# Kernel tuning notes

Hardware: AMD Instinct MI355X
Metric: run time of the kernel (lower is better)

## Reference

```python
import jax, jax.numpy as jnp
import numpy as np

D_MODEL = 1024
NUM_HEADS = 16
D_K = D_MODEL // NUM_HEADS
NEG_INF = -1.0e9


def setup_inputs() -> dict:
    key = jax.random.key(0)
    ks = jax.random.split(key, 12)
    B, S = 2, 2048
    s = 1.0 / np.sqrt(D_MODEL)
    return {
        "q": jax.random.normal(ks[0], (B, S, D_MODEL), jnp.float32),
        "k": jax.random.normal(ks[1], (B, S, D_MODEL), jnp.float32),
        "v": jax.random.normal(ks[2], (B, S, D_MODEL), jnp.float32),
        "encoder_mask": jnp.ones((B, 1, 1, S), jnp.int32),
        "W_q": jax.random.normal(ks[3], (D_MODEL, D_MODEL), jnp.float32) * s,
        "b_q": jnp.zeros((D_MODEL,), jnp.float32),
        "W_k": jax.random.normal(ks[4], (D_MODEL, D_MODEL), jnp.float32) * s,
        "b_k": jnp.zeros((D_MODEL,), jnp.float32),
        "W_v": jax.random.normal(ks[5], (D_MODEL, D_MODEL), jnp.float32) * s,
        "b_v": jnp.zeros((D_MODEL,), jnp.float32),
        "W_o": jax.random.normal(ks[6], (D_MODEL, D_MODEL), jnp.float32) * s,
        "b_o": jnp.zeros((D_MODEL,), jnp.float32),
    }


def reference(q, k, v, encoder_mask, W_q, b_q, W_k, b_k, W_v, b_v, W_o, b_o):
    B, S, _ = q.shape
    # projections (torch Linear: x @ W^T + b)
    def proj(x, W, b):
        y = x @ W.T + b
        return y.reshape(B, -1, NUM_HEADS, D_K).transpose(0, 2, 1, 3)  # [B,H,S,dk]

    Q = proj(q, W_q, b_q)
    K = proj(k, W_k, b_k)
    V = proj(v, W_v, b_v)

    scores = jnp.einsum("bhqd,bhkd->bhqk", Q, K) / jnp.sqrt(jnp.float32(D_K))
    scores = jnp.where(encoder_mask == 0, NEG_INF, scores)
    # NOTE: source module computes softmax(scores) but then (bug) multiplies
    # the raw masked scores by V; softmax result is dead code, so we skip it.
    attn_out = jnp.einsum("bhqk,bhkd->bhqd", scores, V)
    attn_out = attn_out.transpose(0, 2, 1, 3).reshape(B, S, D_MODEL)
    return attn_out @ W_o.T + b_o
```

## Files before the change

### kernel.cpp

```cpp
#include <hip/hip_runtime.h>
#include <stdint.h>

#define DM 1024
#define NH 16
#define DK 64

typedef __attribute__((ext_vector_type(8))) __bf16 bf16x8;
typedef __attribute__((ext_vector_type(4))) float f32x4;

__device__ __forceinline__ float bf2f(unsigned short u) {
    union { uint32_t i; float f; } x; x.i = ((uint32_t)u) << 16; return x.f;
}
__device__ __forceinline__ unsigned short f2bf(float f) {
    union { float f; uint32_t i; } x; x.f = f;
    uint32_t r = x.i + 0x7fffu + ((x.i >> 16) & 1u);
    return (unsigned short)(r >> 16);
}

__device__ __forceinline__ void gl2lds16(const void* g, void* l) {
    __builtin_amdgcn_global_load_lds(
        (const __attribute__((address_space(1))) void*)g,
        (__attribute__((address_space(3))) void*)l, 16, 0, 0);
}

__device__ __forceinline__ f32x4 mfma_bf16(bf16x8 a, bf16x8 b, f32x4 c) {
    return __builtin_amdgcn_mfma_f32_16x16x32_bf16(a, b, c, 0, 0, 0);
}

template<int N> __device__ __forceinline__ void waitvm() {
    if constexpr (N == 0) asm volatile("s_waitcnt vmcnt(0)" ::: "memory");
}

struct CvtArgs {
    const float* src[15];
    unsigned short* dst[15];
};

__global__ __launch_bounds__(256) void cvt15(CvtArgs a) {
    const int t = blockIdx.x * 256 + threadIdx.x;
    const int seg = t >> 18;
    const int off = t & 0x3ffff;
    const float4 v = reinterpret_cast<const float4*>(a.src[seg])[off];
    ushort4 o;
    o.x = f2bf(v.x); o.y = f2bf(v.y); o.z = f2bf(v.z); o.w = f2bf(v.w);
    reinterpret_cast<ushort4*>(a.dst[seg])[off] = o;
}

template<typename OutT>
struct GKArgs {
    const unsigned short* A[3];
    const unsigned short* Wlo[3];
    const unsigned short* Whi[3];
    const float* blo[3];
    const float* bhi[3];
    OutT* C[3];
};

template<int BM, int BN, typename OutT>
__global__ __launch_bounds__(256, 4) void gemmk(GKArgs<OutT> g, int M, int N, int K,
                                                int nwgx, int rowSplit)
{
    constexpr int SA = BM / 64;
    constexpr int SB = BN / 64;
    constexpr int FN = BN / 32;
    constexpr int BUFE = (BM + BN) * 32;
    constexpr int EPIE = BM * BN * (int)(sizeof(OutT) / 2);
    constexpr int LDSE = (2 * BUFE > EPIE) ? 2 * BUFE : EPIE;

    const int z = blockIdx.y;
    const int nwg = gridDim.x;
    const int f = blockIdx.x;
    const int q = nwg >> 3;
    const int f2 = (f & 7) * q + (f >> 3);
    const int bx = f2 % nwgx, by = f2 / nwgx;
    const int row0 = by * BM, col0 = bx * BN;

    const unsigned short* __restrict__ A = g.A[z];
    const bool hi = row0 >= rowSplit;
    const unsigned short* __restrict__ Bw = hi ? g.Whi[z] : g.Wlo[z];
    const float* __restrict__ bias = hi ? g.bhi[z] : g.blo[z];
    OutT* __restrict__ C = g.C[z];

    __shared__ unsigned short lds[LDSE];

    const int tid  = threadIdx.x;
    const int lane = tid & 63;
    const int w    = tid >> 6;
    const int wr   = w >> 1, wc = w & 1;
    const int l15  = lane & 15;
    const int swz  = (l15 & 12) << 2;

    const int tidp = tid ^ ((tid >> 4) & 3);
    const unsigned short* aSrc = A  + (size_t)(row0 + (tidp >> 2)) * K + (tidp & 3) * 8;
    const unsigned short* bSrc = Bw + (size_t)(col0 + (tidp >> 2)) * K + (tidp & 3) * 8;

    const int aBase = (((wr * 64 + l15) * 64) + (lane >> 4) * 16) ^ swz;
    const int bBase = (((wc * (BN / 2) + l15) * 64) + (lane >> 4) * 16) ^ swz;

    f32x4 acc[4][FN];
    #pragma unroll
    for (int m = 0; m < 4; ++m)
        #pragma unroll
        for (int n = 0; n < FN; ++n)
            acc[m][n] = (f32x4){0.f, 0.f, 0.f, 0.f};

    const int NT = K >> 5;

    #define STAGE(t) do { \
        unsigned short* bufE = lds + ((t) & 1) * BUFE; \
        _Pragma("unroll") \
        for (int i = 0; i < SA; ++i) \
            gl2lds16(aSrc + (size_t)(t) * 32 + (size_t)i * 64 * K, \
                     bufE + i * 2048 + tid * 8); \
        _Pragma("unroll") \
        for (int i = 0; i < SB; ++i) \
            gl2lds16(bSrc + (size_t)(t) * 32 + (size_t)i * 64 * K, \
                     bufE + BM * 32 + i * 2048 + tid * 8); \
    } while (0)

    STAGE(0);
    waitvm<0>();
    __builtin_amdgcn_s_barrier();

    #pragma unroll 2
    for (int t = 0; t < NT; ++t) {
        if (t + 1 < NT) STAGE(t + 1);
        const char* LA = (const char*)lds + (t & 1) * (BUFE * 2);
        const char* LB = LA + BM * 64;
        bf16x8 af[4], bfv[FN];
        #pragma unroll
        for (int m = 0; m < 4; ++m)
            af[m] = *reinterpret_cast<const bf16x8*>(LA + m * 1024 + aBase);
        #pragma unroll
        for (int n = 0; n < FN; ++n)
            bfv[n] = *reinterpret_cast<const bf16x8*>(LB + n * 1024 + bBase);
        __builtin_amdgcn_s_setprio(1);
        #pragma unroll
        for (int m = 0; m < 4; ++m)
            #pragma unroll
            for (int n = 0; n < FN; ++n)
                acc[m][n] = mfma_bf16(af[m], bfv[n], acc[m][n]);
        __builtin_amdgcn_s_setprio(0);
        if (t + 1 < NT) waitvm<0>();
        __builtin_amdgcn_s_barrier();
    }
    #undef STAGE

    const int cr = (lane >> 4) * 4, cc = l15;
    if constexpr (sizeof(OutT) == 2) {
        unsigned short* CE = lds;
        #pragma unroll
        for (int n = 0; n < FN; ++n) {
            const int col = wc * (BN / 2) + n * 16 + cc;
            const float bv = bias[col0 + col];
            #pragma unroll
            for (int m = 0; m < 4; ++m) {
                const int rowb = wr * 64 + m * 16 + cr;
                #pragma unroll
                for (int r = 0; r < 4; ++r)
                    CE[(rowb + r) * BN + col] = f2bf(acc[m][n][r] + bv);
            }
        }
        __syncthreads();
        constexpr int NJ = BM * BN * 2 / 4096;
        #pragma unroll
        for (int j = 0; j < NJ; ++j) {
            const int off = j * 4096 + tid * 16;
            const int row = off / (BN * 2);
            const int cole = (off % (BN * 2)) >> 1;
            *reinterpret_cast<uint4*>(&C[(size_t)(row0 + row) * N + col0 + cole]) =
                *reinterpret_cast<const uint4*>((const char*)CE + off);
        }
    } else {
        float* CE = reinterpret_cast<float*>(lds);
        #pragma unroll
        for (int n = 0; n < FN; ++n) {
            const int col = wc * (BN / 2) + n * 16 + cc;
            const float bv = bias[col0 + col];
            #pragma unroll
            for (int m = 0; m < 4; ++m) {
                const int rowb = wr * 64 + m * 16 + cr;
                #pragma unroll
                for (int r = 0; r < 4; ++r)
                    CE[(rowb + r) * BN + col] = acc[m][n][r] + bv;
            }
        }
        __syncthreads();
        constexpr int NJ = BM * BN * 4 / 4096;
        #pragma unroll
        for (int j = 0; j < NJ; ++j) {
            const int off = j * 4096 + tid * 16;
            const int row = off / (BN * 4);
            const int cole = (off % (BN * 4)) >> 2;
            *reinterpret_cast<uint4*>(&C[(size_t)(row0 + row) * N + col0 + cole]) =
                *reinterpret_cast<const uint4*>((const char*)CE + off);
        }
    }
}

__global__ __launch_bounds__(256) void ktv_partial(
    const unsigned short* __restrict__ Kb, const unsigned short* __restrict__ Vb,
    const int* __restrict__ mask, float* __restrict__ Mpart,
    float* __restrict__ cvpart, int S, int schunk)
{
    __shared__ float Ks[16][64];
    __shared__ float Vs[16][64];
    __shared__ float cvs[16][64];
    const int bh = blockIdx.x, chunk = blockIdx.y, BH = gridDim.x;
    const int b = bh >> 4, h = bh & 15;
    const int tid = threadIdx.x;
    const int tx = tid & 15, ty = tid >> 4;
    const int s0 = chunk * schunk;

    float acc[4][4] = {};
    float cv[4] = {0.f, 0.f, 0.f, 0.f};

    for (int sc = 0; sc < schunk; sc += 16) {
        const int s = s0 + sc + ty;
        const size_t rowoff = (size_t)(b * S + s) * DM + h * DK + tx * 4;
        const ushort4 kraw = *reinterpret_cast<const ushort4*>(Kb + rowoff);
        const ushort4 vraw = *reinterpret_cast<const ushort4*>(Vb + rowoff);
        float4 kv = make_float4(bf2f(kraw.x), bf2f(kraw.y), bf2f(kraw.z), bf2f(kraw.w));
        const float4 vv = make_float4(bf2f(vraw.x), bf2f(vraw.y), bf2f(vraw.z), bf2f(vraw.w));
        if (mask[b * S + s] == 0) {
            cv[0] += vv.x; cv[1] += vv.y; cv[2] += vv.z; cv[3] += vv.w;
            kv = make_float4(0.f, 0.f, 0.f, 0.f);
        }
        __syncthreads();
        *reinterpret_cast<float4*>(&Ks[ty][tx * 4]) = kv;
        *reinterpret_cast<float4*>(&Vs[ty][tx * 4]) = vv;
        __syncthreads();
        #pragma unroll
        for (int ss = 0; ss < 16; ++ss) {
            const float4 kq = *reinterpret_cast<const float4*>(&Ks[ss][ty * 4]);
            const float4 vq = *reinterpret_cast<const float4*>(&Vs[ss][tx * 4]);
            const float kvv[4] = {kq.x, kq.y, kq.z, kq.w};
            const float vvv[4] = {vq.x, vq.y, vq.z, vq.w};
            #pragma unroll
            for (int i = 0; i < 4; ++i)
                #pragma unroll
                for (int j = 0; j < 4; ++j)
                    acc[i][j] += kvv[i] * vvv[j];
        }
    }

    const size_t mbase = ((size_t)chunk * BH + bh) * (DK * DK);
    #pragma unroll
    for (int i = 0; i < 4; ++i)
        #pragma unroll
        for (int j = 0; j < 4; ++j)
            Mpart[mbase + (size_t)(ty * 4 + i) * DK + tx * 4 + j] = acc[i][j];

    __syncthreads();
    #pragma unroll
    for (int j = 0; j < 4; ++j) cvs[ty][tx * 4 + j] = cv[j];
    __syncthreads();
    if (tid < DK) {
        float s = 0.f;
        #pragma unroll
        for (int r = 0; r < 16; ++r) s += cvs[r][tid];
        cvpart[((size_t)chunk * BH + bh) * DK + tid] = s;
    }
}

__global__ __launch_bounds__(256) void reduce_m(
    const float* __restrict__ Mpart, const float* __restrict__ cvpart,
    float* __restrict__ Mm, float* __restrict__ cvec, int nchunk, int BH)
{
    const int bh = blockIdx.x;
    const int tid = threadIdx.x;
    const int e0 = blockIdx.y * 512;
    for (int e = e0 + tid; e < e0 + 512; e += 256) {
        float s = 0.f;
        for (int c = 0; c < nchunk; ++c)
            s += Mpart[((size_t)c * BH + bh) * (DK * DK) + e];
        Mm[(size_t)bh * DK * DK + e] = s * 0.125f;
    }
    if (blockIdx.y == 0 && tid < DK) {
        float s = 0.f;
        for (int c = 0; c < nchunk; ++c)
            s += cvpart[((size_t)c * BH + bh) * DK + tid];
        cvec[bh * DK + tid] = s;
    }
}

__device__ __forceinline__ bf16x8 ld_cvt8(const float* p) {
    const float4 x = *reinterpret_cast<const float4*>(p);
    const float4 y = *reinterpret_cast<const float4*>(p + 4);
    union { unsigned short u[8]; bf16x8 v; } r;
    r.u[0] = f2bf(x.x); r.u[1] = f2bf(x.y); r.u[2] = f2bf(x.z); r.u[3] = f2bf(x.w);
    r.u[4] = f2bf(y.x); r.u[5] = f2bf(y.y); r.u[6] = f2bf(y.z); r.u[7] = f2bf(y.w);
    return r.v;
}

__global__ __launch_bounds__(256) void fuse_w(
    const float* __restrict__ Mm, const float* __restrict__ Wo,
    unsigned short* __restrict__ Wf)
{
    const int h = blockIdx.y;
    const int b = blockIdx.z;
    const int o0 = blockIdx.x * 256;
    const int tid = threadIdx.x, lane = tid & 63, w = tid >> 6;
    const int l15 = lane & 15, q8 = (lane >> 4) * 8;
    const float* MmH = Mm + (size_t)(b * NH + h) * (DK * DK);

    f32x4 acc[4][4];
    #pragma unroll
    for (int m = 0; m < 4; ++m)
        #pragma unroll
        for (int n = 0; n < 4; ++n)
            acc[m][n] = (f32x4){0.f, 0.f, 0.f, 0.f};

    bf16x8 af[4][2], bf[4][2];
    #pragma unroll
    for (int m = 0; m < 4; ++m) {
        const int orow = o0 + w * 64 + m * 16 + l15;
        #pragma unroll
        for (int kk = 0; kk < 2; ++kk)
            af[m][kk] = ld_cvt8(Wo + (size_t)orow * DM + h * DK + kk * 32 + q8);
    }
    #pragma unroll
    for (int n = 0; n < 4; ++n) {
        const int d = n * 16 + l15;
        #pragma unroll
        for (int kk = 0; kk < 2; ++kk)
            bf[n][kk] = ld_cvt8(MmH + (size_t)d * DK + kk * 32 + q8);
    }
    #pragma unroll
    for (int kk = 0; kk < 2; ++kk)
        #pragma unroll
        for (int m = 0; m < 4; ++m)
            #pragma unroll
            for (int n = 0; n < 4; ++n)
                acc[m][n] = mfma_bf16(af[m][kk], bf[n][kk], acc[m][n]);

    const int cr = (lane >> 4) * 4, cc = lane & 15;
    #pragma unroll
    for (int n = 0; n < 4; ++n)
        #pragma unroll
        for (int m = 0; m < 4; ++m)
            #pragma unroll
            for (int r = 0; r < 4; ++r)
                Wf[(size_t)b * DM * DM +
                   (size_t)(o0 + w * 64 + m * 16 + cr + r) * DM +
                   h * DK + n * 16 + cc] = f2bf(acc[m][n][r]);
}

__global__ __launch_bounds__(256) void fuse_bias(
    const float* __restrict__ cvec, const float* __restrict__ Wo,
    const float* __restrict__ bo, float* __restrict__ bias2)
{
    const int w = threadIdx.x >> 6, lane = threadIdx.x & 63;
    const int o = blockIdx.x * 4 + w;
    const float* wr = Wo + (size_t)o * DM + lane * 16;
    const float* c0 = cvec + lane * 16;
    const float* c1 = cvec + DM + lane * 16;
    float s0 = 0.f, s1 = 0.f;
    #pragma unroll
    for (int u = 0; u < 4; ++u) {
        const float4 w4 = *reinterpret_cast<const float4*>(wr + u * 4);
        const float4 a4 = *reinterpret_cast<const float4*>(c0 + u * 4);
        const float4 b4 = *reinterpret_cast<const float4*>(c1 + u * 4);
        s0 += w4.x * a4.x + w4.y * a4.y + w4.z * a4.z + w4.w * a4.w;
        s1 += w4.x * b4.x + w4.y * b4.y + w4.z * b4.z + w4.w * b4.w;
    }
    #pragma unroll
    for (int d = 32; d >= 1; d >>= 1) {
        s0 += __shfl_xor(s0, d, 64);
        s1 += __shfl_xor(s1, d, 64);
    }
    if (lane == 0) {
        const float bv = bo[o];
        bias2[o]      = bv - 1.0e9f * s0;
        bias2[DM + o] = bv - 1.0e9f * s1;
    }
}

extern "C" void kernel_launch(void* const* d_in, const int* in_sizes, int n_in,
                              void* d_out, int out_size, void* d_ws, size_t ws_size,
                              hipStream_t stream)
{
    const float* q    = (const float*)d_in[0];
    const float* k    = (const float*)d_in[1];
    const float* v    = (const float*)d_in[2];
    const int*   mask = (const int*)  d_in[3];
    const float* Wq   = (const float*)d_in[4];
    const float* bq   = (const float*)d_in[5];
    const float* Wk   = (const float*)d_in[6];
    const float* bk   = (const float*)d_in[7];
    const float* Wv   = (const float*)d_in[8];
    const float* bv   = (const float*)d_in[9];
    const float* Wo   = (const float*)d_in[10];
    const float* bo   = (const float*)d_in[11];
    float* out = (float*)d_out;

    const int BS = in_sizes[0] / DM;
    const int B  = 2;
    const int S  = BS / B;
    const int BH = B * NH;
    const int SCHUNK = 64;
    const int NCHUNK = S / SCHUNK;
    const size_t BSDM = (size_t)BS * DM;
    const size_t DMDM = (size_t)DM * DM;

    unsigned short* ws = (unsigned short*)d_ws;
    unsigned short* qb   = ws;
    unsigned short* kb   = qb  + BSDM;
    unsigned short* vb   = kb  + BSDM;
    unsigned short* Wqb  = vb  + BSDM;
    unsigned short* Wkb  = Wqb + DMDM;
    unsigned short* Wvb  = Wkb + DMDM;
    unsigned short* Qp   = Wvb + DMDM;
    unsigned short* Kp   = Qp  + BSDM;
    unsigned short* Vp   = Kp  + BSDM;
    float* Mpart = (float*)kb;
    float* cvprt = (float*)Wqb;
    float* Mm    = cvprt + (size_t)NCHUNK * BH * DK;
    float* cvec  = Mm    + (size_t)BH * DK * DK;
    unsigned short* Wf = qb;
    float* bias2 = (float*)Wkb;

    const dim3 blk(256);

    CvtArgs cv;
    for (int i = 0; i < 4; ++i) { cv.src[0 + i] = q + (size_t)i * DMDM; cv.dst[0 + i] = qb + (size_t)i * DMDM; }
    for (int i = 0; i < 4; ++i) { cv.src[4 + i] = k + (size_t)i * DMDM; cv.dst[4 + i] = kb + (size_t)i * DMDM; }
    for (int i = 0; i < 4; ++i) { cv.src[8 + i] = v + (size_t)i * DMDM; cv.dst[8 + i] = vb + (size_t)i * DMDM; }
    cv.src[12] = Wq; cv.dst[12] = Wqb;
    cv.src[13] = Wk; cv.dst[13] = Wkb;
    cv.src[14] = Wv; cv.dst[14] = Wvb;
    cvt15<<<dim3(15 * 1024), blk, 0, stream>>>(cv);

    GKArgs<unsigned short> ga;
    ga.A[0] = qb;  ga.A[1] = kb;  ga.A[2] = vb;
    ga.Wlo[0] = ga.Whi[0] = Wqb;
    ga.Wlo[1] = ga.Whi[1] = Wkb;
    ga.Wlo[2] = ga.Whi[2] = Wvb;
    ga.blo[0] = ga.bhi[0] = bq;
    ga.blo[1] = ga.bhi[1] = bk;
    ga.blo[2] = ga.bhi[2] = bv;
    ga.C[0] = Qp;  ga.C[1] = Kp;  ga.C[2] = Vp;
    gemmk<128, 128, unsigned short>
        <<<dim3((DM / 128) * (BS / 128), 3), blk, 0, stream>>>(
        ga, BS, DM, DM, DM / 128, 1 << 30);

    ktv_partial<<<dim3(BH, NCHUNK), blk, 0, stream>>>(Kp, Vp, mask, Mpart, cvprt, S, SCHUNK);
    reduce_m<<<dim3(BH, 8), blk, 0, stream>>>(Mpart, cvprt, Mm, cvec, NCHUNK, BH);

    fuse_w<<<dim3(DM / 256, NH, B), blk, 0, stream>>>(Mm, Wo, Wf);
    fuse_bias<<<dim3(DM / 4), blk, 0, stream>>>(cvec, Wo, bo, bias2);

    GKArgs<float> gf;
    gf.A[0] = Qp;
    gf.Wlo[0] = Wf;        gf.Whi[0] = Wf + DMDM;
    gf.blo[0] = bias2;     gf.bhi[0] = bias2 + DM;
    gf.C[0] = out;
    gf.A[1] = gf.A[2] = nullptr;
    gf.Wlo[1] = gf.Wlo[2] = gf.Whi[1] = gf.Whi[2] = nullptr;
    gf.blo[1] = gf.blo[2] = gf.bhi[1] = gf.bhi[2] = nullptr;
    gf.C[1] = gf.C[2] = nullptr;
    gemmk<128, 64, float>
        <<<dim3((DM / 64) * (BS / 128), 1), blk, 0, stream>>>(
        gf, BS, DM, DM, DM / 64, S);
}
```

Measured before the change: 118.9 us.

## Fuse fp32-to-bf16 activation conversion into QKV projection GEMM A-tile staging

The separate conversion pass over q, k and v is removed. The QKV GEMM now streams fp32 activations straight into LDS with a new swizzle and converts them to bf16 when loading fragments. This avoids writing and re-reading a bf16 copy of the activations, but it doubles the A-tile LDS footprint and global read bytes per tile and adds conversion ALU work in the inner loop. Occupancy launch bounds drop from 4 to 3, and the workspace layout is reorganised.

```diff
diff --git a/kernel.cpp b/kernel.cpp
--- a/kernel.cpp
+++ b/kernel.cpp
@@ -32,11 +32,11 @@
 }
 
 struct CvtArgs {
-    const float* src[15];
-    unsigned short* dst[15];
+    const float* src[3];
+    unsigned short* dst[3];
 };
 
-__global__ __launch_bounds__(256) void cvt15(CvtArgs a) {
+__global__ __launch_bounds__(256) void cvt3(CvtArgs a) {
     const int t = blockIdx.x * 256 + threadIdx.x;
     const int seg = t >> 18;
     const int off = t & 0x3ffff;
@@ -48,7 +48,7 @@
 
 template<typename OutT>
 struct GKArgs {
-    const unsigned short* A[3];
+    const void* A[3];
     const unsigned short* Wlo[3];
     const unsigned short* Whi[3];
     const float* blo[3];
@@ -56,16 +56,17 @@
     OutT* C[3];
 };
 
-template<int BM, int BN, typename OutT>
-__global__ __launch_bounds__(256, 4) void gemmk(GKArgs<OutT> g, int M, int N, int K,
+template<int BM, int BN, bool F32A, typename OutT>
+__global__ __launch_bounds__(256, 3) void gemmk(GKArgs<OutT> g, int M, int N, int K,
                                                 int nwgx, int rowSplit)
 {
-    constexpr int SA = BM / 64;
+    static_assert(!F32A || BM == 128, "F32A staging hardcodes BM=128");
     constexpr int SB = BN / 64;
     constexpr int FN = BN / 32;
-    constexpr int BUFE = (BM + BN) * 32;
-    constexpr int EPIE = BM * BN * (int)(sizeof(OutT) / 2);
-    constexpr int LDSE = (2 * BUFE > EPIE) ? 2 * BUFE : EPIE;
+    constexpr int ABYTES = F32A ? BM * 128 : BM * 64;
+    constexpr int BUFE   = ABYTES / 2 + BN * 32;
+    constexpr int EPIE   = BM * BN * (int)(sizeof(OutT) / 2);
+    constexpr int LDSE   = (2 * BUFE > EPIE) ? 2 * BUFE : EPIE;
 
     const int z = blockIdx.y;
     const int nwg = gridDim.x;
@@ -75,7 +76,6 @@
     const int bx = f2 % nwgx, by = f2 / nwgx;
     const int row0 = by * BM, col0 = bx * BN;
 
-    const unsigned short* __restrict__ A = g.A[z];
     const bool hi = row0 >= rowSplit;
     const unsigned short* __restrict__ Bw = hi ? g.Whi[z] : g.Wlo[z];
     const float* __restrict__ bias = hi ? g.bhi[z] : g.blo[z];
@@ -91,10 +91,19 @@
     const int swz  = (l15 & 12) << 2;
 
     const int tidp = tid ^ ((tid >> 4) & 3);
-    const unsigned short* aSrc = A  + (size_t)(row0 + (tidp >> 2)) * K + (tidp & 3) * 8;
     const unsigned short* bSrc = Bw + (size_t)(col0 + (tidp >> 2)) * K + (tidp & 3) * 8;
 
-    const int aBase = (((wr * 64 + l15) * 64) + (lane >> 4) * 16) ^ swz;
+    const float* aSrcF = nullptr;
+    const unsigned short* aSrcH = nullptr;
+    if constexpr (F32A)
+        aSrcF = (const float*)g.A[z]
+              + (size_t)(row0 + (tid >> 3)) * K
+              + (size_t)(((tid & 7) ^ ((tid >> 3) & 7)) * 4);
+    else
+        aSrcH = (const unsigned short*)g.A[z] + (size_t)(row0 + (tidp >> 2)) * K + (tidp & 3) * 8;
+
+    const int aB0f = (((wr * 64 + l15) * 128) + (lane >> 4) * 32) ^ ((l15 & 7) << 4);
+    const int aB0h = (((wr * 64 + l15) * 64) + (lane >> 4) * 16) ^ swz;
     const int bBase = (((wc * (BN / 2) + l15) * 64) + (lane >> 4) * 16) ^ swz;
 
     f32x4 acc[4][FN];
@@ -108,14 +117,21 @@
 
     #define STAGE(t) do { \
         unsigned short* bufE = lds + ((t) & 1) * BUFE; \
+        if constexpr (F32A) { \
+            _Pragma("unroll") \
+            for (int i_ = 0; i_ < 4; ++i_) \
+                gl2lds16(aSrcF + (size_t)(t) * 32 + (size_t)i_ * 32 * K, \
+                         bufE + i_ * 2048 + tid * 8); \
+        } else { \
+            _Pragma("unroll") \
+            for (int i_ = 0; i_ < BM / 64; ++i_) \
+                gl2lds16(aSrcH + (size_t)(t) * 32 + (size_t)i_ * 64 * K, \
+                         bufE + i_ * 2048 + tid * 8); \
+        } \
         _Pragma("unroll") \
-        for (int i = 0; i < SA; ++i) \
-            gl2lds16(aSrc + (size_t)(t) * 32 + (size_t)i * 64 * K, \
-                     bufE + i * 2048 + tid * 8); \
-        _Pragma("unroll") \
-        for (int i = 0; i < SB; ++i) \
-            gl2lds16(bSrc + (size_t)(t) * 32 + (size_t)i * 64 * K, \
-                     bufE + BM * 32 + i * 2048 + tid * 8); \
+        for (int i_ = 0; i_ < SB; ++i_) \
+            gl2lds16(bSrc + (size_t)(t) * 32 + (size_t)i_ * 64 * K, \
+                     bufE + ABYTES / 2 + i_ * 2048 + tid * 8); \
     } while (0)
 
     STAGE(0);
@@ -125,15 +141,30 @@
     #pragma unroll 2
     for (int t = 0; t < NT; ++t) {
         if (t + 1 < NT) STAGE(t + 1);
-        const char* LA = (const char*)lds + (t & 1) * (BUFE * 2);
-        const char* LB = LA + BM * 64;
+        const char* LAb = (const char*)lds + (t & 1) * (BUFE * 2);
+        const char* LBb = LAb + ABYTES;
         bf16x8 af[4], bfv[FN];
-        #pragma unroll
-        for (int m = 0; m < 4; ++m)
-            af[m] = *reinterpret_cast<const bf16x8*>(LA + m * 1024 + aBase);
+        if constexpr (F32A) {
+            #pragma unroll
+            for (int m = 0; m < 4; ++m) {
+                const int b0 = m * 2048 + aB0f;
+                const float4 f0 = *reinterpret_cast<const float4*>(LAb + b0);
+                const float4 f1 = *reinterpret_cast<const float4*>(LAb + (b0 ^ 16));
+                union { unsigned short u[8]; bf16x8 v; } r_;
+                r_.u[0] = f2bf(f0.x); r_.u[1] = f2bf(f0.y);
+                r_.u[2] = f2bf(f0.z); r_.u[3] = f2bf(f0.w);
+                r_.u[4] = f2bf(f1.x); r_.u[5] = f2bf(f1.y);
+                r_.u[6] = f2bf(f1.z); r_.u[7] = f2bf(f1.w);
+                af[m] = r_.v;
+            }
+        } else {
+            #pragma unroll
+            for (int m = 0; m < 4; ++m)
+                af[m] = *reinterpret_cast<const bf16x8*>(LAb + m * 1024 + aB0h);
+        }
         #pragma unroll
         for (int n = 0; n < FN; ++n)
-            bfv[n] = *reinterpret_cast<const bf16x8*>(LB + n * 1024 + bBase);
+            bfv[n] = *reinterpret_cast<const bf16x8*>(LBb + n * 1024 + bBase);
         __builtin_amdgcn_s_setprio(1);
         #pragma unroll
         for (int m = 0; m < 4; ++m)
@@ -404,35 +435,29 @@
     const size_t DMDM = (size_t)DM * DM;
 
     unsigned short* ws = (unsigned short*)d_ws;
-    unsigned short* qb   = ws;
-    unsigned short* kb   = qb  + BSDM;
-    unsigned short* vb   = kb  + BSDM;
-    unsigned short* Wqb  = vb  + BSDM;
-    unsigned short* Wkb  = Wqb + DMDM;
-    unsigned short* Wvb  = Wkb + DMDM;
-    unsigned short* Qp   = Wvb + DMDM;
-    unsigned short* Kp   = Qp  + BSDM;
-    unsigned short* Vp   = Kp  + BSDM;
-    float* Mpart = (float*)kb;
-    float* cvprt = (float*)Wqb;
+    unsigned short* Wqb = ws;
+    unsigned short* Wkb = Wqb + DMDM;
+    unsigned short* Wvb = Wkb + DMDM;
+    unsigned short* Qp  = Wvb + DMDM;
+    unsigned short* Kp  = Qp + BSDM;
+    unsigned short* Vp  = Kp + BSDM;
+    float* Mpart = (float*)(Vp + BSDM);
+    float* cvprt = Mpart + (size_t)NCHUNK * BH * DK * DK;
     float* Mm    = cvprt + (size_t)NCHUNK * BH * DK;
-    float* cvec  = Mm    + (size_t)BH * DK * DK;
-    unsigned short* Wf = qb;
-    float* bias2 = (float*)Wkb;
+    float* cvec  = Mm + (size_t)BH * DK * DK;
+    float* bias2 = cvec + (size_t)B * DM;
+    unsigned short* Wf = (unsigned short*)Mpart;
 
     const dim3 blk(256);
 
     CvtArgs cv;
-    for (int i = 0; i < 4; ++i) { cv.src[0 + i] = q + (size_t)i * DMDM; cv.dst[0 + i] = qb + (size_t)i * DMDM; }
-    for (int i = 0; i < 4; ++i) { cv.src[4 + i] = k + (size_t)i * DMDM; cv.dst[4 + i] = kb + (size_t)i * DMDM; }
-    for (int i = 0; i < 4; ++i) { cv.src[8 + i] = v + (size_t)i * DMDM; cv.dst[8 + i] = vb + (size_t)i * DMDM; }
-    cv.src[12] = Wq; cv.dst[12] = Wqb;
-    cv.src[13] = Wk; cv.dst[13] = Wkb;
-    cv.src[14] = Wv; cv.dst[14] = Wvb;
-    cvt15<<<dim3(15 * 1024), blk, 0, stream>>>(cv);
+    cv.src[0] = Wq; cv.dst[0] = Wqb;
+    cv.src[1] = Wk; cv.dst[1] = Wkb;
+    cv.src[2] = Wv; cv.dst[2] = Wvb;
+    cvt3<<<dim3(3 * 1024), blk, 0, stream>>>(cv);
 
     GKArgs<unsigned short> ga;
-    ga.A[0] = qb;  ga.A[1] = kb;  ga.A[2] = vb;
+    ga.A[0] = q;   ga.A[1] = k;   ga.A[2] = v;
     ga.Wlo[0] = ga.Whi[0] = Wqb;
     ga.Wlo[1] = ga.Whi[1] = Wkb;
     ga.Wlo[2] = ga.Whi[2] = Wvb;
@@ -440,7 +465,7 @@
     ga.blo[1] = ga.bhi[1] = bk;
     ga.blo[2] = ga.bhi[2] = bv;
     ga.C[0] = Qp;  ga.C[1] = Kp;  ga.C[2] = Vp;
-    gemmk<128, 128, unsigned short>
+    gemmk<128, 128, true, unsigned short>
         <<<dim3((DM / 128) * (BS / 128), 3), blk, 0, stream>>>(
         ga, BS, DM, DM, DM / 128, 1 << 30);
 
@@ -459,7 +484,7 @@
     gf.Wlo[1] = gf.Wlo[2] = gf.Whi[1] = gf.Whi[2] = nullptr;
     gf.blo[1] = gf.blo[2] = gf.bhi[1] = gf.bhi[2] = nullptr;
     gf.C[1] = gf.C[2] = nullptr;
-    gemmk<128, 64, float>
+    gemmk<128, 64, false, float>
         <<<dim3((DM / 64) * (BS / 128), 1), blk, 0, stream>>>(
         gf, BS, DM, DM, DM / 64, S);
 }
```

Result: no change. 119.5 us (+0.5%).
